# Optimization experiments

Measured on AMD Instinct MI355X. Metric: run time of the kernel, lower is better.

## Reference

```python
import jax, jax.numpy as jnp
import numpy as np

EPS = 1e-07
BETA = 1.0
NEG_INF = -1e30


def setup_inputs() -> dict:
    key = jax.random.key(0)
    k1, k2 = jax.random.split(key)
    B, C = 262144, 128
    inputs = jax.random.normal(k1, (B, C), dtype=jnp.float32)
    targets = jax.random.randint(k2, (B,), 0, C, dtype=jnp.int64)
    return {"inputs": inputs, "targets": targets}


def reference(inputs, targets):
    B, C = inputs.shape
    dt = inputs.dtype
    probs = jax.nn.sigmoid(inputs)  # (B, C)

    # per-class counts (size_class in torch code)
    counts = jax.ops.segment_sum(jnp.ones((B,), dtype=dt), targets, num_segments=C)  # (C,)
    present = counts > 0
    safe_counts = jnp.where(present, counts, jnp.asarray(1.0, dt))

    # per-class mean of probs over samples with that label -> rows of mean_probs
    sum_probs = jax.ops.segment_sum(probs, targets, num_segments=C)  # (C, C)
    mean_probs = sum_probs / safe_counts[:, None]
    diag = jnp.arange(C)
    mean_probs = mean_probs.at[diag, diag].set(-1.0)  # mean_probs_k[k] = -1

    # positive term: mean over class-k samples of log(p[i,k]+eps), summed over present classes
    logp_pos_true = jnp.log(jnp.take_along_axis(probs, targets[:, None], axis=1)[:, 0] + EPS)  # (B,)
    pos_per_class = jax.ops.segment_sum(logp_pos_true, targets, num_segments=C) / safe_counts
    loss_pos = jnp.sum(jnp.where(present, pos_per_class, jnp.asarray(0.0, dt)))

    # per-class mean of log(1-p+eps) with the true-class column zeroed ((1-onehot) factor)
    logp_neg = jnp.log(1.0 - probs + EPS)  # (B, C)
    sum_logneg = jax.ops.segment_sum(logp_neg, targets, num_segments=C)  # (C, C)
    mean_loss_neg = (sum_logneg / safe_counts[:, None]).at[diag, diag].set(0.0)

    # negative term: per column k, softmax over present rows j != k of beta*mean_probs[j,k]
    mask = present[:, None] & (~jnp.eye(C, dtype=bool))  # rows j, cols k
    logits = jnp.where(mask, BETA * mean_probs, jnp.asarray(NEG_INF, dt))
    weights = jax.nn.softmax(logits, axis=0) * mask.astype(dt)  # zero weight when column fully masked
    loss_neg = jnp.sum(weights * mean_loss_neg)

    return -1.0 * (loss_pos + loss_neg)
```

## Files before the change

### kernel.cpp

```cpp
#include <hip/hip_runtime.h>
#include <math.h>

#define C      128
#define CAPLG  12
#define CAP    (1 << CAPLG)
#define SPLIT  16
#define SPB    1024
#define REDN   (2*C*C + 2*C)
#define PBS    260
#define LN2F   0.69314718056f

__device__ __forceinline__ float fast_rcp(float x) { return __builtin_amdgcn_rcpf(x); }

__global__ __launch_bounds__(256)
void scatter_kernel(const int* __restrict__ tgt, int* __restrict__ cursor,
                    int* __restrict__ perm, int B) {
    __shared__ int lcur[C];
    __shared__ int sbase[C];
    if (threadIdx.x < C) lcur[threadIdx.x] = 0;
    __syncthreads();
    const int base = blockIdx.x * SPB;
    int myt[SPB / 256], myr[SPB / 256];
#pragma unroll
    for (int j = 0; j < SPB / 256; ++j) {
        int i = base + j * 256 + threadIdx.x;
        if (i < B) { myt[j] = tgt[i]; myr[j] = atomicAdd(&lcur[myt[j]], 1); }
        else myt[j] = -1;
    }
    __syncthreads();
    if (threadIdx.x < C) sbase[threadIdx.x] = atomicAdd(&cursor[threadIdx.x], lcur[threadIdx.x]);
    __syncthreads();
#pragma unroll
    for (int j = 0; j < SPB / 256; ++j)
        if (myt[j] >= 0)
            perm[(myt[j] << CAPLG) + sbase[myt[j]] + myr[j]] = base + j * 256 + threadIdx.x;
}

__global__ __launch_bounds__(256)
void main_kernel(const float* __restrict__ x, const int* __restrict__ perm,
                 const int* __restrict__ cursor, float* __restrict__ partial) {
    const int k = blockIdx.x / SPLIT;
    const int p = blockIdx.x % SPLIT;
    const int n = min(cursor[k], CAP);
    const int chunk = (n + SPLIT - 1) / SPLIT;
    const int s0 = min(p * chunk, n);
    const int s1 = min(s0 + chunk, n);

    const int tid  = threadIdx.x;
    const int wave = tid >> 6;
    const int lane = tid & 63;
    const int half = lane >> 5;
    const int l5   = lane & 31;
    const int c0   = l5 << 2;
    const bool poslane = (l5 == (k >> 2));
    const int  ksub = k & 3;

    const int wlen = (s1 - s0 + 3) >> 2;
    const int ws0  = s0 + wave * wlen;
    const int ws1  = min(ws0 + wlen, s1);

    const int* bperm = perm + (k << CAPLG);

    float ap0=0,ap1=0,ap2=0,ap3=0;
    float sx0=0,sx1=0,sx2=0,sx3=0;
    float sl0=0,sl1=0,sl2=0,sl3=0;
    float apos = 0.f;

    for (int tbase = ws0; tbase < ws1; tbase += 64) {
        const int tl = min(64, ws1 - tbase);
        const int pv = (lane < tl) ? bperm[tbase + lane] : 0;
        const int h  = (tl + 1) >> 1;
        int iA = __shfl(pv, 0);
        int iB = __shfl(pv, (h < tl) ? h : 0);
        float4 cur = *reinterpret_cast<const float4*>(
                         x + (size_t)(half ? iB : iA) * C + c0);
        for (int j = 0; j < h; ++j) {
            float4 nxt = cur;
            if (j + 1 < h) {
                int nA = __shfl(pv, j + 1);
                int nB = __shfl(pv, (j + 1 + h < tl) ? j + 1 + h : j + 1);
                nxt = *reinterpret_cast<const float4*>(
                          x + (size_t)(half ? nB : nA) * C + c0);
            }
            const bool valid = (half == 0) || (j + h < tl);
            if (valid) {
                float e, u, lu0, lu1, lu2, lu3;
                e = __expf(-cur.x); u = 1.f + e; lu0 = __log2f(u);
                ap0 += fast_rcp(u); sx0 += cur.x; sl0 += lu0;
                e = __expf(-cur.y); u = 1.f + e; lu1 = __log2f(u);
                ap1 += fast_rcp(u); sx1 += cur.y; sl1 += lu1;
                e = __expf(-cur.z); u = 1.f + e; lu2 = __log2f(u);
                ap2 += fast_rcp(u); sx2 += cur.z; sl2 += lu2;
                e = __expf(-cur.w); u = 1.f + e; lu3 = __log2f(u);
                ap3 += fast_rcp(u); sx3 += cur.w; sl3 += lu3;
                if (poslane) {
                    float lsel = (ksub & 2) ? ((ksub & 1) ? lu3 : lu2)
                                            : ((ksub & 1) ? lu1 : lu0);
                    apos += lsel;
                }
            }
            cur = nxt;
        }
    }

    __shared__ __align__(16) float sP[8][C];
    __shared__ __align__(16) float sX[8][C];
    __shared__ __align__(16) float sL[8][C];
    __shared__ float sPos[8];
    const int g = (wave << 1) | half;
    *reinterpret_cast<float4*>(&sP[g][c0]) = make_float4(ap0, ap1, ap2, ap3);
    *reinterpret_cast<float4*>(&sX[g][c0]) = make_float4(sx0, sx1, sx2, sx3);
    *reinterpret_cast<float4*>(&sL[g][c0]) = make_float4(sl0, sl1, sl2, sl3);
    if (poslane) sPos[g] = apos;
    __syncthreads();

    float* mine = partial + (size_t)blockIdx.x * PBS;
    if (tid < C) {
        float s = 0.f;
#pragma unroll
        for (int g2 = 0; g2 < 8; ++g2) s += sP[g2][tid];
        mine[tid] = s;
    } else {
        const int t = tid - C;
        float sx = 0.f, sl = 0.f;
#pragma unroll
        for (int g2 = 0; g2 < 8; ++g2) { sx += sX[g2][t]; sl += sL[g2][t]; }
        mine[C + t] = -sx - LN2F * sl;
    }
    if (tid == 0) {
        float s = 0.f;
#pragma unroll
        for (int g2 = 0; g2 < 8; ++g2) s += sPos[g2];
        mine[256] = -LN2F * s;
    }
}

__global__ __launch_bounds__(256)
void reduce2_kernel(const float* __restrict__ partial, const int* __restrict__ cursor,
                    float* __restrict__ red) {
    const int k = blockIdx.x;
    const int t = threadIdx.x;
    float s = 0.f;
#pragma unroll
    for (int p = 0; p < SPLIT; ++p)
        s += partial[(size_t)(k * SPLIT + p) * PBS + t];
    if (t < C) red[k * C + t] = s;
    else       red[C * C + k * C + (t - C)] = s;
    if (t == 0) {
        float ps = 0.f;
#pragma unroll
        for (int p = 0; p < SPLIT; ++p)
            ps += partial[(size_t)(k * SPLIT + p) * PBS + 256];
        red[2 * C * C + C + k] = ps;
        red[2 * C * C + k]     = (float)cursor[k];
    }
}

__global__ __launch_bounds__(64)
void finalize_col_kernel(const float* __restrict__ red, float* __restrict__ colpart) {
    const float* sp  = red;
    const float* sln = red + C * C;
    const float* cnt = red + 2 * C * C;
    const float* pos = red + 2 * C * C + C;

    const int k = blockIdx.x;
    const int l = threadIdx.x;
    const int j0 = l, j1 = l + 64;

    const float c0 = cnt[j0], c1 = cnt[j1];
    const bool  v0 = (j0 != k) && (c0 > 0.f);
    const bool  v1 = (j1 != k) && (c1 > 0.f);

    const float x0 = v0 ? sp[j0 * C + k] / c0 : -INFINITY;
    const float x1 = v1 ? sp[j1 * C + k] / c1 : -INFINITY;

    float m = fmaxf(x0, x1);
#pragma unroll
    for (int d = 1; d < 64; d <<= 1) m = fmaxf(m, __shfl_xor(m, d));

    float w0 = v0 ? __expf(x0 - m) : 0.f;
    float w1 = v1 ? __expf(x1 - m) : 0.f;
    float den = w0 + w1;
    float num = (v0 ? w0 * (sln[j0 * C + k] / c0) : 0.f)
              + (v1 ? w1 * (sln[j1 * C + k] / c1) : 0.f);
#pragma unroll
    for (int d = 1; d < 64; d <<= 1) { den += __shfl_xor(den, d); num += __shfl_xor(num, d); }

    if (l == 0) {
        float colneg = (den > 0.f) ? num / den : 0.f;
        float ck     = cnt[k];
        float pk     = (ck > 0.f) ? pos[k] / ck : 0.f;
        colpart[k]   = colneg + pk;
    }
}

__global__ __launch_bounds__(64)
void finalize_sum_kernel(const float* __restrict__ colpart, float* __restrict__ out) {
    const int l = threadIdx.x;
    float s = colpart[l] + colpart[l + 64];
#pragma unroll
    for (int d = 1; d < 64; d <<= 1) s += __shfl_xor(s, d);
    if (l == 0) out[0] = -s;
}

extern "C" void kernel_launch(void* const* d_in, const int* in_sizes, int n_in,
                              void* d_out, int out_size, void* d_ws, size_t ws_size,
                              hipStream_t stream) {
    const float* x   = (const float*)d_in[0];
    const int*   tgt = (const int*)d_in[1];
    const int B = in_sizes[1];

    int*   cursor  = (int*)d_ws;
    int*   perm    = cursor + C;
    float* partial = (float*)(perm + C * CAP);
    float* red     = partial + (size_t)(C * SPLIT) * PBS;
    float* colpart = red + REDN;

    hipMemsetAsync(cursor, 0, C * sizeof(int), stream);
    scatter_kernel<<<(B + SPB - 1) / SPB, 256, 0, stream>>>(tgt, cursor, perm, B);
    main_kernel<<<C * SPLIT, 256, 0, stream>>>(x, perm, cursor, partial);
    reduce2_kernel<<<C, 256, 0, stream>>>(partial, cursor, red);
    finalize_col_kernel<<<C, 64, 0, stream>>>(red, colpart);
    finalize_sum_kernel<<<1, 64, 0, stream>>>(colpart, (float*)d_out);
}
```

Before: 48.26 us.

## Fuse reduce and finalize kernels, transpose partials, pad cursors, deepen prefetch

After: 50.70 us. +5.0%, slower.

```diff
diff --git a/kernel.cpp b/kernel.cpp
--- a/kernel.cpp
+++ b/kernel.cpp
@@ -5,15 +5,15 @@
 #define CAPLG  12
 #define CAP    (1 << CAPLG)
 #define SPLIT  16
+#define NMB    (C * SPLIT)
 #define SPB    1024
-#define REDN   (2*C*C + 2*C)
-#define PBS    260
+#define CSTR   16
 #define LN2F   0.69314718056f
 
 __device__ __forceinline__ float fast_rcp(float x) { return __builtin_amdgcn_rcpf(x); }
 
 __global__ __launch_bounds__(256)
-void scatter_kernel(const int* __restrict__ tgt, int* __restrict__ cursor,
+void scatter_kernel(const int* __restrict__ tgt, int* __restrict__ cursor2,
                     int* __restrict__ perm, int B) {
     __shared__ int lcur[C];
     __shared__ int sbase[C];
@@ -28,7 +28,8 @@
         else myt[j] = -1;
     }
     __syncthreads();
-    if (threadIdx.x < C) sbase[threadIdx.x] = atomicAdd(&cursor[threadIdx.x], lcur[threadIdx.x]);
+    if (threadIdx.x < C)
+        sbase[threadIdx.x] = atomicAdd(&cursor2[threadIdx.x * CSTR], lcur[threadIdx.x]);
     __syncthreads();
 #pragma unroll
     for (int j = 0; j < SPB / 256; ++j)
@@ -38,10 +39,10 @@
 
 __global__ __launch_bounds__(256)
 void main_kernel(const float* __restrict__ x, const int* __restrict__ perm,
-                 const int* __restrict__ cursor, float* __restrict__ partial) {
+                 const int* __restrict__ cursor2, float* __restrict__ partial) {
     const int k = blockIdx.x / SPLIT;
     const int p = blockIdx.x % SPLIT;
-    const int n = min(cursor[k], CAP);
+    const int n = min(cursor2[k * CSTR], CAP);
     const int chunk = (n + SPLIT - 1) / SPLIT;
     const int s0 = min(p * chunk, n);
     const int s1 = min(s0 + chunk, n);
@@ -70,17 +71,22 @@
         const int tl = min(64, ws1 - tbase);
         const int pv = (lane < tl) ? bperm[tbase + lane] : 0;
         const int h  = (tl + 1) >> 1;
+
         int iA = __shfl(pv, 0);
         int iB = __shfl(pv, (h < tl) ? h : 0);
-        float4 cur = *reinterpret_cast<const float4*>(
-                         x + (size_t)(half ? iB : iA) * C + c0);
+        float4 cur = *reinterpret_cast<const float4*>(x + (size_t)(half ? iB : iA) * C + c0);
+        float4 nxt = cur;
+        if (h > 1) {
+            iA = __shfl(pv, 1);
+            iB = __shfl(pv, (1 + h < tl) ? 1 + h : 1);
+            nxt = *reinterpret_cast<const float4*>(x + (size_t)(half ? iB : iA) * C + c0);
+        }
         for (int j = 0; j < h; ++j) {
-            float4 nxt = cur;
-            if (j + 1 < h) {
-                int nA = __shfl(pv, j + 1);
-                int nB = __shfl(pv, (j + 1 + h < tl) ? j + 1 + h : j + 1);
-                nxt = *reinterpret_cast<const float4*>(
-                          x + (size_t)(half ? nB : nA) * C + c0);
+            float4 fut = cur;
+            if (j + 2 < h) {
+                iA = __shfl(pv, j + 2);
+                iB = __shfl(pv, (j + 2 + h < tl) ? j + 2 + h : j + 2);
+                fut = *reinterpret_cast<const float4*>(x + (size_t)(half ? iB : iA) * C + c0);
             }
             const bool valid = (half == 0) || (j + h < tl);
             if (valid) {
@@ -99,7 +105,7 @@
                     apos += lsel;
                 }
             }
-            cur = nxt;
+            cur = nxt; nxt = fut;
         }
     }
 
@@ -114,93 +120,95 @@
     if (poslane) sPos[g] = apos;
     __syncthreads();
 
-    float* mine = partial + (size_t)blockIdx.x * PBS;
+    const int bq = blockIdx.x;
     if (tid < C) {
         float s = 0.f;
 #pragma unroll
         for (int g2 = 0; g2 < 8; ++g2) s += sP[g2][tid];
-        mine[tid] = s;
+        partial[(size_t)tid * NMB + bq] = s;
     } else {
         const int t = tid - C;
         float sx = 0.f, sl = 0.f;
 #pragma unroll
         for (int g2 = 0; g2 < 8; ++g2) { sx += sX[g2][t]; sl += sL[g2][t]; }
-        mine[C + t] = -sx - LN2F * sl;
+        partial[(size_t)(C + t) * NMB + bq] = -sx - LN2F * sl;
     }
     if (tid == 0) {
         float s = 0.f;
 #pragma unroll
         for (int g2 = 0; g2 < 8; ++g2) s += sPos[g2];
-        mine[256] = -LN2F * s;
+        partial[(size_t)(2 * C) * NMB + bq] = -LN2F * s;
     }
 }
 
 __global__ __launch_bounds__(256)
-void reduce2_kernel(const float* __restrict__ partial, const int* __restrict__ cursor,
-                    float* __restrict__ red) {
-    const int k = blockIdx.x;
-    const int t = threadIdx.x;
-    float s = 0.f;
-#pragma unroll
-    for (int p = 0; p < SPLIT; ++p)
-        s += partial[(size_t)(k * SPLIT + p) * PBS + t];
-    if (t < C) red[k * C + t] = s;
-    else       red[C * C + k * C + (t - C)] = s;
-    if (t == 0) {
-        float ps = 0.f;
-#pragma unroll
-        for (int p = 0; p < SPLIT; ++p)
-            ps += partial[(size_t)(k * SPLIT + p) * PBS + 256];
-        red[2 * C * C + C + k] = ps;
-        red[2 * C * C + k]     = (float)cursor[k];
-    }
-}
-
-__global__ __launch_bounds__(64)
-void finalize_col_kernel(const float* __restrict__ red, float* __restrict__ colpart) {
-    const float* sp  = red;
-    const float* sln = red + C * C;
-    const float* cnt = red + 2 * C * C;
-    const float* pos = red + 2 * C * C + C;
-
-    const int k = blockIdx.x;
-    const int l = threadIdx.x;
-    const int j0 = l, j1 = l + 64;
-
-    const float c0 = cnt[j0], c1 = cnt[j1];
-    const bool  v0 = (j0 != k) && (c0 > 0.f);
-    const bool  v1 = (j1 != k) && (c1 > 0.f);
-
-    const float x0 = v0 ? sp[j0 * C + k] / c0 : -INFINITY;
-    const float x1 = v1 ? sp[j1 * C + k] / c1 : -INFINITY;
-
-    float m = fmaxf(x0, x1);
-#pragma unroll
-    for (int d = 1; d < 64; d <<= 1) m = fmaxf(m, __shfl_xor(m, d));
-
-    float w0 = v0 ? __expf(x0 - m) : 0.f;
-    float w1 = v1 ? __expf(x1 - m) : 0.f;
-    float den = w0 + w1;
-    float num = (v0 ? w0 * (sln[j0 * C + k] / c0) : 0.f)
-              + (v1 ? w1 * (sln[j1 * C + k] / c1) : 0.f);
-#pragma unroll
-    for (int d = 1; d < 64; d <<= 1) { den += __shfl_xor(den, d); num += __shfl_xor(num, d); }
-
-    if (l == 0) {
-        float colneg = (den > 0.f) ? num / den : 0.f;
-        float ck     = cnt[k];
-        float pk     = (ck > 0.f) ? pos[k] / ck : 0.f;
-        colpart[k]   = colneg + pk;
-    }
-}
-
-__global__ __launch_bounds__(64)
-void finalize_sum_kernel(const float* __restrict__ colpart, float* __restrict__ out) {
-    const int l = threadIdx.x;
-    float s = colpart[l] + colpart[l + 64];
-#pragma unroll
-    for (int d = 1; d < 64; d <<= 1) s += __shfl_xor(s, d);
-    if (l == 0) out[0] = -s;
+void finalize_kernel(const float* __restrict__ partial, const int* __restrict__ cursor2,
+                     float* __restrict__ colpart, int* __restrict__ ticket,
+                     float* __restrict__ out) {
+    const int k   = blockIdx.x;
+    const int tid = threadIdx.x;
+
+    __shared__ float spcol[C], slcol[C];
+    __shared__ float sposr[16];
+
+    {
+        const int j    = tid >> 1;
+        const int base = j * SPLIT + (tid & 1) * 8;
+        const float4* rp = reinterpret_cast<const float4*>(partial + (size_t)k * NMB + base);
+        const float4* rl = reinterpret_cast<const float4*>(partial + (size_t)(C + k) * NMB + base);
+        float4 a = rp[0], b = rp[1];
+        float accP = a.x + a.y + a.z + a.w + b.x + b.y + b.z + b.w;
+        a = rl[0]; b = rl[1];
+        float accL = a.x + a.y + a.z + a.w + b.x + b.y + b.z + b.w;
+        accP += __shfl_xor(accP, 1);
+        accL += __shfl_xor(accL, 1);
+        if ((tid & 1) == 0) { spcol[j] = accP; slcol[j] = accL; }
+        if (tid < SPLIT) sposr[tid] = partial[(size_t)(2 * C) * NMB + k * SPLIT + tid];
+    }
+    __syncthreads();
+
+    if (tid < 64) {
+        const int l = tid, j0 = l, j1 = l + 64;
+        const float c0 = (float)cursor2[j0 * CSTR];
+        const float c1 = (float)cursor2[j1 * CSTR];
+        const bool  v0 = (j0 != k) && (c0 > 0.f);
+        const bool  v1 = (j1 != k) && (c1 > 0.f);
+        const float x0 = v0 ? spcol[j0] / c0 : -INFINITY;
+        const float x1 = v1 ? spcol[j1] / c1 : -INFINITY;
+
+        float m = fmaxf(x0, x1);
+#pragma unroll
+        for (int d = 1; d < 64; d <<= 1) m = fmaxf(m, __shfl_xor(m, d));
+
+        float w0 = v0 ? __expf(x0 - m) : 0.f;
+        float w1 = v1 ? __expf(x1 - m) : 0.f;
+        float den = w0 + w1;
+        float num = (v0 ? w0 * (slcol[j0] / c0) : 0.f)
+                  + (v1 ? w1 * (slcol[j1] / c1) : 0.f);
+#pragma unroll
+        for (int d = 1; d < 64; d <<= 1) { den += __shfl_xor(den, d); num += __shfl_xor(num, d); }
+
+        int last = 0;
+        if (l == 0) {
+            float colneg = (den > 0.f) ? num / den : 0.f;
+            float ck     = (float)cursor2[k * CSTR];
+            float ps     = 0.f;
+#pragma unroll
+            for (int q = 0; q < SPLIT; ++q) ps += sposr[q];
+            float pk = (ck > 0.f) ? ps / ck : 0.f;
+            colpart[k] = colneg + pk;
+            __threadfence();
+            last = (atomicAdd(ticket, 1) == C - 1);
+        }
+        last = __shfl(last, 0);
+        if (last) {
+            __threadfence();
+            float s = colpart[l] + colpart[l + 64];
+#pragma unroll
+            for (int d = 1; d < 64; d <<= 1) s += __shfl_xor(s, d);
+            if (l == 0) out[0] = -s;
+        }
+    }
 }
 
 extern "C" void kernel_launch(void* const* d_in, const int* in_sizes, int n_in,
@@ -210,16 +218,14 @@
     const int*   tgt = (const int*)d_in[1];
     const int B = in_sizes[1];
 
-    int*   cursor  = (int*)d_ws;
-    int*   perm    = cursor + C;
+    int*   cursor2 = (int*)d_ws;
+    int*   ticket  = cursor2 + C * CSTR;
+    int*   perm    = cursor2 + C * CSTR + CSTR;
     float* partial = (float*)(perm + C * CAP);
-    float* red     = partial + (size_t)(C * SPLIT) * PBS;
-    float* colpart = red + REDN;
-
-    hipMemsetAsync(cursor, 0, C * sizeof(int), stream);
-    scatter_kernel<<<(B + SPB - 1) / SPB, 256, 0, stream>>>(tgt, cursor, perm, B);
-    main_kernel<<<C * SPLIT, 256, 0, stream>>>(x, perm, cursor, partial);
-    reduce2_kernel<<<C, 256, 0, stream>>>(partial, cursor, red);
-    finalize_col_kernel<<<C, 64, 0, stream>>>(red, colpart);
-    finalize_sum_kernel<<<1, 64, 0, stream>>>(colpart, (float*)d_out);
-}
+    float* colpart = partial + (size_t)(2 * C + 1) * NMB;
+
+    hipMemsetAsync(cursor2, 0, (C * CSTR + CSTR) * sizeof(int), stream);
+    scatter_kernel<<<(B + SPB - 1) / SPB, 256, 0, stream>>>(tgt, cursor2, perm, B);
+    main_kernel<<<NMB, 256, 0, stream>>>(x, perm, cursor2, partial);
+    finalize_kernel<<<C, 256, 0, stream>>>(partial, cursor2, colpart, ticket, (float*)d_out);
+}
```
